# Kernel tuning notes

Measured on AMD Instinct MI355X. Metric: run time of the kernel, lower is better.

Reference implementation:

```python
import jax, jax.numpy as jnp
import numpy as np

B, N, D, H = 4, 2048, 512, 8
HD = D // H


def setup_inputs() -> dict:
    key = jax.random.key(0)
    ks = jax.random.split(key, 12)
    s = 1.0 / np.sqrt(D)
    return {
        "node_feat": jax.random.normal(ks[0], (B, N, D), jnp.float32),
        "edge_weights": jax.random.uniform(ks[1], (B, N, N), jnp.float32),
        "adj_matrix": jax.random.uniform(ks[2], (B, N, N), jnp.float32),
        "masks": jnp.ones((B, N), jnp.float32),
        "class_token": 0.02 * jax.random.normal(ks[3], (1, 1, D), jnp.float32),
        "Wq": jax.random.uniform(ks[4], (D, D), jnp.float32, -s, s),
        "bq": jnp.zeros((D,), jnp.float32),
        "Wk": jax.random.uniform(ks[5], (D, D), jnp.float32, -s, s),
        "bk": jnp.zeros((D,), jnp.float32),
        "Wv": jax.random.uniform(ks[6], (D, D), jnp.float32, -s, s),
        "bv": jnp.zeros((D,), jnp.float32),
        "Wo": jax.random.uniform(ks[7], (D, D), jnp.float32, -s, s),
        "bo": jnp.zeros((D,), jnp.float32),
        "gamma": jnp.ones((D,), jnp.float32),
        "beta": jnp.zeros((D,), jnp.float32),
    }


def _attn_mask(edge_weights, masks):
    # inner block: edge gates + self-loops, clamped at 1
    inner = jnp.minimum(edge_weights + jnp.eye(N, dtype=edge_weights.dtype), 1.0)
    top = jnp.concatenate([jnp.ones((B, 1, 1), edge_weights.dtype), masks[:, None, :]], axis=2)  # [B,1,1+N]
    bot = jnp.concatenate([jnp.ones((B, N, 1), edge_weights.dtype), inner], axis=2)              # [B,N,1+N]
    m = jnp.concatenate([top, bot], axis=1)  # [B,1+N,1+N]
    ext = jnp.concatenate([jnp.ones((B, 1), masks.dtype), masks], axis=1)  # [B,1+N], CLS always valid
    return m * ext[:, None, :] * ext[:, :, None]


def reference(node_feat, edge_weights, adj_matrix, masks, class_token,
              Wq, bq, Wk, bk, Wv, bv, Wo, bo, gamma, beta):
    x = jnp.concatenate([jnp.broadcast_to(class_token, (B, 1, D)), node_feat], axis=1)  # [B,1+N,D]
    S = 1 + N
    q = (x @ Wq.T + bq).reshape(B, S, H, HD).transpose(0, 2, 1, 3)
    k = (x @ Wk.T + bk).reshape(B, S, H, HD).transpose(0, 2, 1, 3)
    v = (x @ Wv.T + bv).reshape(B, S, H, HD).transpose(0, 2, 1, 3)
    scores = jnp.einsum('bhqd,bhkd->bhqk', q, k) / jnp.sqrt(jnp.float32(HD))
    m = _attn_mask(edge_weights, masks)
    scores = jnp.where(m[:, None, :, :] == 0, jnp.float32(-1e9), scores)
    attn = jax.nn.softmax(scores, axis=-1)
    out = jnp.einsum('bhqk,bhkd->bhqd', attn, v).transpose(0, 2, 1, 3).reshape(B, S, D)
    out = out @ Wo.T + bo
    y = out + x
    mu = jnp.mean(y, axis=-1, keepdims=True)
    var = jnp.mean((y - mu) ** 2, axis=-1, keepdims=True)
    y = (y - mu) / jnp.sqrt(var + 1e-5) * gamma + beta
    return y[:, 0, :]
```

## Files before the change

### kernel.cpp

```cpp
#include <hip/hip_runtime.h>

#define B_ 4
#define N_ 2048
#define D_ 512
#define H_ 8
#define S_ (N_ + 1)
#define SC 32
#define NCH 65

#define Q0_OFF   0
#define TQ_OFF   1024
#define ATTN_OFF 8192
#define PW_OFF   81920
#define PZ_OFF   (PW_OFF + NCH * B_ * H_ * D_)
#define W_OFF    (PZ_OFF + NCH * B_ * H_ + 32)
#define O0_OFF   (W_OFF + B_ * H_ * D_)
#define Y_OFF    (O0_OFF + B_ * D_)

__device__ __forceinline__ float wave_reduce_sum(float v) {
    #pragma unroll
    for (int off = 32; off > 0; off >>= 1) v += __shfl_down(v, off, 64);
    return v;
}
__device__ __forceinline__ float wave_allreduce_sum(float v) {
    #pragma unroll
    for (int off = 1; off < 64; off <<= 1) v += __shfl_xor(v, off, 64);
    return v;
}

__global__ void q0_kernel(const float* __restrict__ ct,
                          const float* __restrict__ Wq, const float* __restrict__ bq,
                          float* __restrict__ ws) {
    int wv = threadIdx.x >> 6, lane = threadIdx.x & 63;
    int r = blockIdx.x * 8 + wv;
    const float4* c4 = (const float4*)ct;
    float4 ca = c4[lane * 2], cb = c4[lane * 2 + 1];
    const float4* row = (const float4*)(Wq + (size_t)r * D_);
    float4 a = row[lane * 2], b = row[lane * 2 + 1];
    float acc = a.x*ca.x + a.y*ca.y + a.z*ca.z + a.w*ca.w
              + b.x*cb.x + b.y*cb.y + b.z*cb.z + b.w*cb.w;
    acc = wave_reduce_sum(acc);
    if (lane == 0) ws[Q0_OFF + r] = acc + bq[r];
}

__global__ void tq_kernel(const float* __restrict__ Wk, float* __restrict__ ws) {
    int h = blockIdx.x, jc = blockIdx.y;
    int tid = threadIdx.x;
    __shared__ float q0s[64];
    if (tid < 64) q0s[tid] = ws[Q0_OFF + h * 64 + tid];
    __syncthreads();
    int j = jc * 128 + tid;
    float acc = 0.f;
    #pragma unroll 8
    for (int d2 = 0; d2 < 64; ++d2)
        acc += q0s[d2] * Wk[(size_t)(h * 64 + d2) * D_ + j];
    ws[TQ_OFF + h * D_ + j] = acc;
}

__global__ void __launch_bounds__(512)
scores_kernel(const float* __restrict__ nf, const float* __restrict__ ct,
              const float* __restrict__ masks, float* __restrict__ ws) {
    int b = blockIdx.y;
    int wv = threadIdx.x >> 6, lane = threadIdx.x & 63;
    int s = blockIdx.x * 8 + wv;
    if (s >= S_) return;
    const float* xrow = (s == 0) ? ct : (nf + ((size_t)b * N_ + (s - 1)) * D_);
    const float4* x4 = (const float4*)xrow;
    float4 xa = x4[lane];
    float4 xb = x4[64 + lane];
    float gate = 1.0f;
    if (s > 0) gate = (masks[b * N_ + s - 1] != 0.0f) ? 1.0f : 0.0f;
    const float4* t4 = (const float4*)(ws + TQ_OFF);
    float p[H_];
    #pragma unroll
    for (int h = 0; h < H_; ++h) {
        float4 ta = t4[h * 128 + lane], tb = t4[h * 128 + 64 + lane];
        p[h] = ta.x*xa.x + ta.y*xa.y + ta.z*xa.z + ta.w*xa.w
             + tb.x*xb.x + tb.y*xb.y + tb.z*xb.z + tb.w*xb.w;
        p[h] = wave_allreduce_sum(p[h]);
    }
    if (lane == 0) {
        #pragma unroll
        for (int h = 0; h < H_; ++h)
            ws[ATTN_OFF + (size_t)(b * H_ + h) * S_ + s] = gate * __expf(p[h] * 0.125f);
    }
}

__global__ void __launch_bounds__(512)
wsum_kernel(const float* __restrict__ nf, const float* __restrict__ ct,
            float* __restrict__ ws) {
    int chunk = blockIdx.x, b = blockIdx.y;
    int tid = threadIdx.x;
    __shared__ float sa[H_][SC];
    int s0 = chunk * SC;
    if (tid < H_ * SC) {
        int h = tid >> 5, ss = tid & 31;
        int s = s0 + ss;
        sa[h][ss] = (s < S_) ? ws[ATTN_OFF + (size_t)(b * H_ + h) * S_ + s] : 0.f;
    }
    __syncthreads();
    float acc[H_];
    #pragma unroll
    for (int h = 0; h < H_; ++h) acc[h] = 0.f;
    int smax = min(SC, S_ - s0);
    for (int ss = 0; ss < smax; ++ss) {
        int s = s0 + ss;
        const float* xrow = (s == 0) ? ct : (nf + ((size_t)b * N_ + (s - 1)) * D_);
        float xv = xrow[tid];
        #pragma unroll
        for (int h = 0; h < H_; ++h) acc[h] += sa[h][ss] * xv;
    }
    size_t base = ((size_t)chunk * B_ + b) * H_;
    #pragma unroll
    for (int h = 0; h < H_; ++h)
        ws[PW_OFF + (base + h) * D_ + tid] = acc[h];
    if (tid < H_) {
        float z = 0.f;
        #pragma unroll 8
        for (int ss = 0; ss < SC; ++ss) z += sa[tid][ss];
        ws[PZ_OFF + base + tid] = z;
    }
}

__global__ void reduce_w_kernel(float* __restrict__ ws) {
    int bh = blockIdx.x;
    int j = blockIdx.y * 128 + threadIdx.x;
    float z = 0.f;
    #pragma unroll 5
    for (int c = 0; c < NCH; ++c) z += ws[PZ_OFF + (size_t)(c * B_ * H_) + bh];
    float acc = 0.f;
    #pragma unroll 5
    for (int c = 0; c < NCH; ++c)
        acc += ws[PW_OFF + ((size_t)(c * B_ * H_) + bh) * D_ + j];
    ws[W_OFF + (size_t)bh * D_ + j] = acc / z;
}

__global__ void wv_kernel(const float* __restrict__ Wv, const float* __restrict__ bv,
                          float* __restrict__ ws) {
    int b = blockIdx.x;
    int wv = threadIdx.x >> 6, lane = threadIdx.x & 63;
    int r = blockIdx.y * 4 + wv;
    const float4* wrow = (const float4*)(ws + W_OFF + (size_t)b * H_ * D_ + (size_t)(r >> 6) * D_);
    float4 wa = wrow[lane * 2], wb = wrow[lane * 2 + 1];
    const float4* row = (const float4*)(Wv + (size_t)r * D_);
    float4 a = row[lane * 2], c = row[lane * 2 + 1];
    float acc = a.x*wa.x + a.y*wa.y + a.z*wa.z + a.w*wa.w
              + c.x*wb.x + c.y*wb.y + c.z*wb.z + c.w*wb.w;
    acc = wave_reduce_sum(acc);
    if (lane == 0) ws[O0_OFF + b * D_ + r] = acc + bv[r];
}

__global__ void wo_kernel(const float* __restrict__ Wo, const float* __restrict__ bo,
                          const float* __restrict__ ct, float* __restrict__ ws) {
    int b = blockIdx.x;
    int wv = threadIdx.x >> 6, lane = threadIdx.x & 63;
    int r = blockIdx.y * 4 + wv;
    const float4* ov = (const float4*)(ws + O0_OFF + (size_t)b * D_);
    float4 oa = ov[lane * 2], ob = ov[lane * 2 + 1];
    const float4* row = (const float4*)(Wo + (size_t)r * D_);
    float4 a = row[lane * 2], c = row[lane * 2 + 1];
    float acc = a.x*oa.x + a.y*oa.y + a.z*oa.z + a.w*oa.w
              + c.x*ob.x + c.y*ob.y + c.z*ob.z + c.w*ob.w;
    acc = wave_reduce_sum(acc);
    if (lane == 0) ws[Y_OFF + b * D_ + r] = acc + bo[r] + ct[r];
}

__global__ void ln_kernel(const float* __restrict__ gamma, const float* __restrict__ beta,
                          const float* __restrict__ ws, float* __restrict__ out) {
    int b = blockIdx.x;
    int tid = threadIdx.x, wv = tid >> 6, lane = tid & 63;
    float v = ws[Y_OFF + b * D_ + tid];
    float s1 = v, s2 = v * v;
    #pragma unroll
    for (int off = 32; off > 0; off >>= 1) {
        s1 += __shfl_down(s1, off, 64);
        s2 += __shfl_down(s2, off, 64);
    }
    __shared__ float r1[8], r2[8];
    if (lane == 0) { r1[wv] = s1; r2[wv] = s2; }
    __syncthreads();
    if (tid == 0) {
        float a = 0.f, c = 0.f;
        for (int i = 0; i < 8; ++i) { a += r1[i]; c += r2[i]; }
        r1[0] = a; r2[0] = c;
    }
    __syncthreads();
    float mean = r1[0] * (1.0f / D_);
    float var  = r2[0] * (1.0f / D_) - mean * mean;
    float rinv = rsqrtf(var + 1e-5f);
    out[b * D_ + tid] = (v - mean) * rinv * gamma[tid] + beta[tid];
}

extern "C" void kernel_launch(void* const* d_in, const int* in_sizes, int n_in,
                              void* d_out, int out_size, void* d_ws, size_t ws_size,
                              hipStream_t stream) {
    const float* nf    = (const float*)d_in[0];
    const float* masks = (const float*)d_in[3];
    const float* ct    = (const float*)d_in[4];
    const float* Wq    = (const float*)d_in[5];
    const float* bq    = (const float*)d_in[6];
    const float* Wk    = (const float*)d_in[7];
    const float* Wv    = (const float*)d_in[9];
    const float* bv    = (const float*)d_in[10];
    const float* Wo    = (const float*)d_in[11];
    const float* bo    = (const float*)d_in[12];
    const float* gamma = (const float*)d_in[13];
    const float* beta  = (const float*)d_in[14];
    float* ws  = (float*)d_ws;
    float* out = (float*)d_out;

    hipLaunchKernelGGL(q0_kernel, dim3(64), dim3(512), 0, stream, ct, Wq, bq, ws);
    hipLaunchKernelGGL(tq_kernel, dim3(H_, 4), dim3(128), 0, stream, Wk, ws);
    hipLaunchKernelGGL(scores_kernel, dim3(257, B_), dim3(512), 0, stream, nf, ct, masks, ws);
    hipLaunchKernelGGL(wsum_kernel, dim3(NCH, B_), dim3(512), 0, stream, nf, ct, ws);
    hipLaunchKernelGGL(reduce_w_kernel, dim3(B_ * H_, 4), dim3(128), 0, stream, ws);
    hipLaunchKernelGGL(wv_kernel, dim3(B_, 128), dim3(256), 0, stream, Wv, bv, ws);
    hipLaunchKernelGGL(wo_kernel, dim3(B_, 128), dim3(256), 0, stream, Wo, bo, ct, ws);
    hipLaunchKernelGGL(ln_kernel, dim3(B_), dim3(512), 0, stream, gamma, beta, ws, out);
}
```

Before: 190.3 us.

## Fuse score computation into weighted-sum kernel via LDS-staged rows; merge q0 into tq

The score kernel and the weighted-sum kernel are merged. Each block stages its 32 node rows into shared memory, computes the gated exp scores for the class query there, then accumulates the weighted sums from the same staged rows. This removes the second global read of node features, the attention-score round trip through the workspace, and one launch. The q0 projection is also folded into the tq kernel, so each head block recomputes its own 64 query entries and another launch goes away. The cost is 64KB of shared memory per block with launch bounds set to one block per CU, which reduces latency hiding.

Result: slower. 208.4 us (+9.5%).

```diff
diff --git a/kernel.cpp b/kernel.cpp
--- a/kernel.cpp
+++ b/kernel.cpp
@@ -10,8 +10,7 @@
 
 #define Q0_OFF   0
 #define TQ_OFF   1024
-#define ATTN_OFF 8192
-#define PW_OFF   81920
+#define PW_OFF   8192
 #define PZ_OFF   (PW_OFF + NCH * B_ * H_ * D_)
 #define W_OFF    (PZ_OFF + NCH * B_ * H_ + 32)
 #define O0_OFF   (W_OFF + B_ * H_ * D_)
@@ -28,75 +27,90 @@
     return v;
 }
 
-__global__ void q0_kernel(const float* __restrict__ ct,
+__global__ void tq_kernel(const float* __restrict__ ct,
                           const float* __restrict__ Wq, const float* __restrict__ bq,
-                          float* __restrict__ ws) {
-    int wv = threadIdx.x >> 6, lane = threadIdx.x & 63;
-    int r = blockIdx.x * 8 + wv;
-    const float4* c4 = (const float4*)ct;
+                          const float* __restrict__ Wk, float* __restrict__ ws) {
+    int h = blockIdx.x, jc = blockIdx.y;
+    int tid = threadIdx.x, wv = tid >> 6, lane = tid & 63;
+    __shared__ float ct_sh[D_];
+    __shared__ float q0_sh[64];
+    ct_sh[tid] = ct[tid];
+    ct_sh[tid + 256] = ct[tid + 256];
+    __syncthreads();
+    const float4* c4 = (const float4*)ct_sh;
     float4 ca = c4[lane * 2], cb = c4[lane * 2 + 1];
-    const float4* row = (const float4*)(Wq + (size_t)r * D_);
-    float4 a = row[lane * 2], b = row[lane * 2 + 1];
-    float acc = a.x*ca.x + a.y*ca.y + a.z*ca.z + a.w*ca.w
-              + b.x*cb.x + b.y*cb.y + b.z*cb.z + b.w*cb.w;
-    acc = wave_reduce_sum(acc);
-    if (lane == 0) ws[Q0_OFF + r] = acc + bq[r];
-}
-
-__global__ void tq_kernel(const float* __restrict__ Wk, float* __restrict__ ws) {
-    int h = blockIdx.x, jc = blockIdx.y;
-    int tid = threadIdx.x;
-    __shared__ float q0s[64];
-    if (tid < 64) q0s[tid] = ws[Q0_OFF + h * 64 + tid];
-    __syncthreads();
-    int j = jc * 128 + tid;
+    #pragma unroll 1
+    for (int rr = 0; rr < 16; ++rr) {
+        int rl = wv * 16 + rr;
+        int r = h * 64 + rl;
+        const float4* row = (const float4*)(Wq + (size_t)r * D_);
+        float4 a = row[lane * 2], b = row[lane * 2 + 1];
+        float acc = a.x*ca.x + a.y*ca.y + a.z*ca.z + a.w*ca.w
+                  + b.x*cb.x + b.y*cb.y + b.z*cb.z + b.w*cb.w;
+        acc = wave_reduce_sum(acc);
+        if (lane == 0) q0_sh[rl] = acc + bq[r];
+    }
+    __syncthreads();
+    int j = jc * 256 + tid;
     float acc = 0.f;
-    #pragma unroll 8
+    #pragma unroll 4
     for (int d2 = 0; d2 < 64; ++d2)
-        acc += q0s[d2] * Wk[(size_t)(h * 64 + d2) * D_ + j];
+        acc += q0_sh[d2] * Wk[(size_t)(h * 64 + d2) * D_ + j];
     ws[TQ_OFF + h * D_ + j] = acc;
 }
 
-__global__ void __launch_bounds__(512)
-scores_kernel(const float* __restrict__ nf, const float* __restrict__ ct,
-              const float* __restrict__ masks, float* __restrict__ ws) {
-    int b = blockIdx.y;
-    int wv = threadIdx.x >> 6, lane = threadIdx.x & 63;
-    int s = blockIdx.x * 8 + wv;
-    if (s >= S_) return;
-    const float* xrow = (s == 0) ? ct : (nf + ((size_t)b * N_ + (s - 1)) * D_);
-    const float4* x4 = (const float4*)xrow;
-    float4 xa = x4[lane];
-    float4 xb = x4[64 + lane];
-    float gate = 1.0f;
-    if (s > 0) gate = (masks[b * N_ + s - 1] != 0.0f) ? 1.0f : 0.0f;
-    const float4* t4 = (const float4*)(ws + TQ_OFF);
-    float p[H_];
-    #pragma unroll
-    for (int h = 0; h < H_; ++h) {
-        float4 ta = t4[h * 128 + lane], tb = t4[h * 128 + 64 + lane];
-        p[h] = ta.x*xa.x + ta.y*xa.y + ta.z*xa.z + ta.w*xa.w
-             + tb.x*xb.x + tb.y*xb.y + tb.z*xb.z + tb.w*xb.w;
-        p[h] = wave_allreduce_sum(p[h]);
-    }
-    if (lane == 0) {
-        #pragma unroll
-        for (int h = 0; h < H_; ++h)
-            ws[ATTN_OFF + (size_t)(b * H_ + h) * S_ + s] = gate * __expf(p[h] * 0.125f);
-    }
-}
-
-__global__ void __launch_bounds__(512)
-wsum_kernel(const float* __restrict__ nf, const float* __restrict__ ct,
-            float* __restrict__ ws) {
+__global__ void __launch_bounds__(512, 1)
+attn_wsum_kernel(const float* __restrict__ nf, const float* __restrict__ ct,
+                 const float* __restrict__ masks, float* __restrict__ ws) {
     int chunk = blockIdx.x, b = blockIdx.y;
-    int tid = threadIdx.x;
+    int tid = threadIdx.x, wv = tid >> 6, lane = tid & 63;
+    __shared__ float xs[SC][D_];
     __shared__ float sa[H_][SC];
     int s0 = chunk * SC;
-    if (tid < H_ * SC) {
-        int h = tid >> 5, ss = tid & 31;
-        int s = s0 + ss;
-        sa[h][ss] = (s < S_) ? ws[ATTN_OFF + (size_t)(b * H_ + h) * S_ + s] : 0.f;
+    float4* xs4 = (float4*)xs;
+    #pragma unroll
+    for (int i = 0; i < 8; ++i) {
+        int f4idx = i * 512 + tid;
+        int row = f4idx >> 7, col = f4idx & 127;
+        int s = s0 + row;
+        if (s < S_) {
+            const float4* src = (s == 0) ? (const float4*)ct
+                                         : (const float4*)(nf + ((size_t)b * N_ + (s - 1)) * D_);
+            xs4[f4idx] = src[col];
+        }
+    }
+    if (tid < H_ * SC) sa[tid >> 5][tid & 31] = 0.f;
+    __syncthreads();
+    {
+        const float4* t4 = (const float4*)(ws + TQ_OFF);
+        float4 tqa[H_], tqb[H_];
+        #pragma unroll
+        for (int h = 0; h < H_; ++h) {
+            tqa[h] = t4[h * 128 + lane];
+            tqb[h] = t4[h * 128 + 64 + lane];
+        }
+        #pragma unroll
+        for (int k = 0; k < 4; ++k) {
+            int row = wv * 4 + k;
+            int s = s0 + row;
+            if (s >= S_) break;
+            const float4* x4 = (const float4*)xs[row];
+            float4 xa = x4[lane], xb = x4[64 + lane];
+            float gate = 1.0f;
+            if (s > 0) gate = (masks[b * N_ + s - 1] != 0.0f) ? 1.0f : 0.0f;
+            float p[H_];
+            #pragma unroll
+            for (int h = 0; h < H_; ++h) {
+                p[h] = tqa[h].x*xa.x + tqa[h].y*xa.y + tqa[h].z*xa.z + tqa[h].w*xa.w
+                     + tqb[h].x*xb.x + tqb[h].y*xb.y + tqb[h].z*xb.z + tqb[h].w*xb.w;
+                p[h] = wave_allreduce_sum(p[h]);
+            }
+            if (lane == 0) {
+                #pragma unroll
+                for (int h = 0; h < H_; ++h)
+                    sa[h][row] = gate * __expf(p[h] * 0.125f);
+            }
+        }
     }
     __syncthreads();
     float acc[H_];
@@ -104,9 +118,7 @@
     for (int h = 0; h < H_; ++h) acc[h] = 0.f;
     int smax = min(SC, S_ - s0);
     for (int ss = 0; ss < smax; ++ss) {
-        int s = s0 + ss;
-        const float* xrow = (s == 0) ? ct : (nf + ((size_t)b * N_ + (s - 1)) * D_);
-        float xv = xrow[tid];
+        float xv = xs[ss][tid];
         #pragma unroll
         for (int h = 0; h < H_; ++h) acc[h] += sa[h][ss] * xv;
     }
@@ -209,10 +221,8 @@
     float* ws  = (float*)d_ws;
     float* out = (float*)d_out;
 
-    hipLaunchKernelGGL(q0_kernel, dim3(64), dim3(512), 0, stream, ct, Wq, bq, ws);
-    hipLaunchKernelGGL(tq_kernel, dim3(H_, 4), dim3(128), 0, stream, Wk, ws);
-    hipLaunchKernelGGL(scores_kernel, dim3(257, B_), dim3(512), 0, stream, nf, ct, masks, ws);
-    hipLaunchKernelGGL(wsum_kernel, dim3(NCH, B_), dim3(512), 0, stream, nf, ct, ws);
+    hipLaunchKernelGGL(tq_kernel, dim3(H_, 2), dim3(256), 0, stream, ct, Wq, bq, Wk, ws);
+    hipLaunchKernelGGL(attn_wsum_kernel, dim3(NCH, B_), dim3(512), 0, stream, nf, ct, masks, ws);
     hipLaunchKernelGGL(reduce_w_kernel, dim3(B_ * H_, 4), dim3(128), 0, stream, ws);
     hipLaunchKernelGGL(wv_kernel, dim3(B_, 128), dim3(256), 0, stream, Wv, bv, ws);
     hipLaunchKernelGGL(wo_kernel, dim3(B_, 128), dim3(256), 0, stream, Wo, bo, ct, ws);
```
